# Performance work log

Measured on AMD Instinct MI355X. Metric: run time of the kernel, lower is better.

## Reference

```python
import jax, jax.numpy as jnp
import numpy as np

H = 128          # hidden / embed dim
NH = 4           # attention heads
HD = H // NH     # head dim = 32
MFD = 4          # missile feat dim
FOD = 15         # full obs dim
NEG_SLOPE = 0.01 # LeakyReLU default


def _gru(x_seq, h0, wih, whh, bih, bhh):
    # x_seq: [B,S,H], h0: [B,H]; torch GRU gate math
    def step(h, x):
        gi = x @ wih.T + bih            # [B,3H]
        gh = h @ whh.T + bhh
        i_r, i_z, i_n = jnp.split(gi, 3, axis=-1)
        h_r, h_z, h_n = jnp.split(gh, 3, axis=-1)
        r = jax.nn.sigmoid(i_r + h_r)
        z = jax.nn.sigmoid(i_z + h_z)
        n = jnp.tanh(i_n + r * h_n)
        h_new = (1.0 - z) * n + z * h
        return h_new, h_new
    h_last, outs = jax.lax.scan(step, h0, jnp.swapaxes(x_seq, 0, 1))
    return jnp.swapaxes(outs, 0, 1), h_last  # [B,S,H], [B,H]


def _ln(x, w, b, eps=1e-5):
    mu = jnp.mean(x, axis=-1, keepdims=True)
    var = jnp.var(x, axis=-1, keepdims=True)
    return (x - mu) * jax.lax.rsqrt(var + eps) * w + b


def setup_inputs() -> dict:
    key = jax.random.key(0)
    ks = jax.random.split(key, 24)
    B, S = 4096, 64
    s = 0.02
    p = {
        "obs": jax.random.normal(ks[0], (B, S, FOD), jnp.float32),
        "h0": jnp.zeros((1, B, H), jnp.float32),
        "enc_air_w": jax.random.normal(ks[1], (H, FOD)) * s,
        "enc_air_b": jnp.zeros((H,)),
        "enc_m_w": jax.random.normal(ks[2], (H, MFD)) * s,
        "enc_m_b": jnp.zeros((H,)),
        "gru_wih": jax.random.normal(ks[3], (3 * H, H)) * s,
        "gru_whh": jax.random.normal(ks[4], (3 * H, H)) * s,
        "gru_bih": jnp.zeros((3 * H,)),
        "gru_bhh": jnp.zeros((3 * H,)),
        "qln_w": jnp.ones((H,)), "qln_b": jnp.zeros((H,)),
        "kln_w": jnp.ones((H,)), "kln_b": jnp.zeros((H,)),
        "attn_in_w": jax.random.normal(ks[5], (3 * H, H)) * s,
        "attn_in_b": jnp.zeros((3 * H,)),
        "attn_out_w": jax.random.normal(ks[6], (H, H)) * s,
        "attn_out_b": jnp.zeros((H,)),
        "mlp0_w": jax.random.normal(ks[7], (H, H)) * s,
        "mlp0_b": jnp.zeros((H,)),
        "mlp1_w": jax.random.normal(ks[8], (H, H)) * s,
        "mlp1_b": jnp.zeros((H,)),
        "fco_w": jax.random.normal(ks[9], (1, H)) * s,
        "fco_b": jnp.zeros((1,)),
    }
    return {k: v.astype(jnp.float32) for k, v in p.items()}


def reference(obs, h0, enc_air_w, enc_air_b, enc_m_w, enc_m_b,
              gru_wih, gru_whh, gru_bih, gru_bhh,
              qln_w, qln_b, kln_w, kln_b,
              attn_in_w, attn_in_b, attn_out_w, attn_out_b,
              mlp0_w, mlp0_b, mlp1_w, mlp1_b, fco_w, fco_b):
    B, S, _ = obs.shape
    N = B * S
    # aircraft encoder + GRU with residual
    air_embed = obs @ enc_air_w.T + enc_air_b                      # [B,S,H]
    gru_out, h_last = _gru(air_embed, h0[0], gru_wih, gru_whh, gru_bih, gru_bhh)
    air_feat = (gru_out + air_embed).reshape(N, H)                 # [N,H]
    # missile encoders (shared weights, two missiles)
    m_raw = obs[..., :2 * MFD].reshape(N, 2, MFD)                  # [N,2,4]
    keys_raw = m_raw @ enc_m_w.T + enc_m_b                         # [N,2,H]
    # inactive-missile mask
    inactive = jnp.array([1.0, 0.0, 1.0, 0.0], obs.dtype)
    mask = jnp.all(jnp.isclose(m_raw, inactive, rtol=1e-5, atol=1e-8), axis=-1)  # [N,2]
    # layer norms
    q_n = _ln(air_feat[:, None, :], qln_w, qln_b)                  # [N,1,H]
    k_n = _ln(keys_raw, kln_w, kln_b)                              # [N,2,H]
    # multihead attention (1 query, 2 keys), values are raw keys
    wq, wk, wv = jnp.split(attn_in_w, 3, axis=0)
    bq, bk, bv = jnp.split(attn_in_b, 3, axis=0)
    q = (q_n @ wq.T + bq).reshape(N, 1, NH, HD)
    k = (k_n @ wk.T + bk).reshape(N, 2, NH, HD)
    v = (keys_raw @ wv.T + bv).reshape(N, 2, NH, HD)
    scores = jnp.einsum('nqhd,nkhd->nhqk', q, k) / jnp.sqrt(jnp.float32(HD))
    scores = scores + jnp.where(mask, -jnp.inf, 0.0)[:, None, None, :]
    attn = jax.nn.softmax(scores, axis=-1)                         # [N,NH,1,2]
    ctx = jnp.einsum('nhqk,nkhd->nqhd', attn, v).reshape(N, H)
    attn_out = ctx @ attn_out_w.T + attn_out_b                     # [N,H]
    attn_out = jnp.where(jnp.isnan(attn_out), 0.0, attn_out)       # nan_to_num guard
    combined = air_feat + attn_out
    # MLP head
    h1 = jax.nn.leaky_relu(combined @ mlp0_w.T + mlp0_b, NEG_SLOPE)
    h2 = jax.nn.leaky_relu(h1 @ mlp1_w.T + mlp1_b, NEG_SLOPE)
    val = h2 @ fco_w.T + fco_b                                     # [N,1]
    return val, h_last[None]
```

## Files before the change

kernel.cpp:

```cpp
#include <hip/hip_runtime.h>
#include <math.h>

#define B_   4096
#define S_   64
#define H_   128
#define N_   (B_*S_)

#define WS_WC    0
#define WS_BC    6144
#define WS_WAP   6528
#define WS_WQP   8576
#define WS_SQ    24960
#define WS_EQ    25088
#define WS_KC    25216
#define WS_EK1   25728
#define WS_SK    25856
#define WS_EK2   25984
#define WS_VC    26112
#define WS_VB    26624
#define WS_MV    26752
#define WS_QQ    26756
#define WS_QLIN  26772
#define WS_MBC   26776
#define WS_C0    26777
#define WS_PB    27392
#define WS_WO2T  (WS_PB + 4096)
#define WS_SROW  (WS_PB + 6784)
#define WS_EROW  (WS_PB + 6812)
#define WS_GB    60160
#define WS_AIR   92928

typedef __attribute__((ext_vector_type(8))) short bf16x8;
typedef __attribute__((ext_vector_type(4))) float f32x4;

__device__ __forceinline__ float dot4(float4 a, float4 b){
    return fmaf(a.x,b.x, fmaf(a.y,b.y, fmaf(a.z,b.z, a.w*b.w)));
}
__device__ __forceinline__ unsigned short f2bf(float f){
    union { float f; unsigned u; } v; v.f = f;
    unsigned r = v.u + 0x7FFF + ((v.u >> 16) & 1);
    return (unsigned short)(r >> 16);
}
__device__ __forceinline__ float bf2f(unsigned short u){
    union { unsigned u; float f; } v; v.u = ((unsigned)u) << 16;
    return v.f;
}

__global__ void precompute_kernel(
    const float* __restrict__ enc_air_w, const float* __restrict__ enc_air_b,
    const float* __restrict__ enc_m_w,  const float* __restrict__ enc_m_b,
    const float* __restrict__ gru_wih,  const float* __restrict__ gru_bih,
    const float* __restrict__ qln_w, const float* __restrict__ qln_b,
    const float* __restrict__ kln_w, const float* __restrict__ kln_b,
    const float* __restrict__ attn_in_w, const float* __restrict__ attn_in_b,
    const float* __restrict__ attn_out_w,
    const float* __restrict__ mlp0_w, const float* __restrict__ mlp1_w,
    float* __restrict__ ws)
{
    int i = blockIdx.x*blockDim.x + threadIdx.x;
    if (i < 6144) {
        int o = i>>4, f = i&15; float a = 0.f;
        if (f < 15) for (int k=0;k<128;k++) a = fmaf(gru_wih[o*128+k], enc_air_w[k*15+f], a);
        ws[WS_WC+i] = a;
    } else if (i < 6528) {
        int o = i-6144; float a = gru_bih[o];
        for (int k=0;k<128;k++) a = fmaf(gru_wih[o*128+k], enc_air_b[k], a);
        ws[WS_BC+o] = a;
    } else if (i < 8576) {
        int idx = i-6528; int j = idx>>4, f = idx&15;
        ws[WS_WAP+idx] = (f<15) ? enc_air_w[j*15+f] : 0.f;
    } else if (i < 24960) {
        int idx = i-8576; int o = idx>>7, j = idx&127;
        ws[WS_WQP+idx] = attn_in_w[o*128+j]*qln_w[j];
    } else if (i < 25088) {
        int o = i-24960; float a=0.f;
        for (int j=0;j<128;j++) a = fmaf(attn_in_w[o*128+j], qln_w[j], a);
        ws[WS_SQ+o]=a;
    } else if (i < 25216) {
        int o = i-25088; float a = attn_in_b[o];
        for (int j=0;j<128;j++) a = fmaf(attn_in_w[o*128+j], qln_b[j], a);
        ws[WS_EQ+o]=a;
    } else if (i < 25728) {
        int idx = i-25216; int o = idx>>2, f = idx&3; float a=0.f;
        for (int j=0;j<128;j++) a = fmaf(attn_in_w[(128+o)*128+j]*kln_w[j], enc_m_w[j*4+f], a);
        ws[WS_KC+idx]=a;
    } else if (i < 25856) {
        int o = i-25728; float a=0.f;
        for (int j=0;j<128;j++) a = fmaf(attn_in_w[(128+o)*128+j]*kln_w[j], enc_m_b[j], a);
        ws[WS_EK1+o]=a;
    } else if (i < 25984) {
        int o = i-25856; float a=0.f;
        for (int j=0;j<128;j++) a = fmaf(attn_in_w[(128+o)*128+j], kln_w[j], a);
        ws[WS_SK+o]=a;
    } else if (i < 26112) {
        int o = i-25984; float a = attn_in_b[128+o];
        for (int j=0;j<128;j++) a = fmaf(attn_in_w[(128+o)*128+j], kln_b[j], a);
        ws[WS_EK2+o]=a;
    } else if (i < 26624) {
        int idx = i-26112; int o = idx>>2, f = idx&3; float a=0.f;
        for (int j=0;j<128;j++) a = fmaf(attn_in_w[(256+o)*128+j], enc_m_w[j*4+f], a);
        ws[WS_VC+idx]=a;
    } else if (i < 26752) {
        int o = i-26624; float a = attn_in_b[256+o];
        for (int j=0;j<128;j++) a = fmaf(attn_in_w[(256+o)*128+j], enc_m_b[j], a);
        ws[WS_VB+o]=a;
    } else if (i < 26756) {
        int f = i-26752; float a=0.f;
        for (int j=0;j<128;j++) a += enc_m_w[j*4+f];
        ws[WS_MV+f]=a*(1.f/128.f);
    } else if (i < 26772) {
        int idx = i-26756; int a4 = idx>>2, b4 = idx&3; float a=0.f;
        for (int j=0;j<128;j++) a = fmaf(enc_m_w[j*4+a4], enc_m_w[j*4+b4], a);
        ws[WS_QQ+idx]=a*(1.f/128.f);
    } else if (i < 26776) {
        int f = i-26772; float a=0.f;
        for (int j=0;j<128;j++) a = fmaf(enc_m_b[j], enc_m_w[j*4+f], a);
        ws[WS_QLIN+f]=a*(2.f/128.f);
    } else if (i == 26776) {
        float a=0.f; for (int j=0;j<128;j++) a += enc_m_b[j];
        ws[WS_MBC]=a*(1.f/128.f);
    } else if (i == 26777) {
        float a=0.f; for (int j=0;j<128;j++) a = fmaf(enc_m_b[j], enc_m_b[j], a);
        ws[WS_C0]=a*(1.f/128.f);
    } else if (i >= 32768 && i < 98304) {
        int idx = i - 32768;
        int mm = idx>>14;
        if (mm >= 2) {
            int i8 = idx & 7, l = (idx>>3)&63, p = (idx>>9)&3, wv = (idx>>11)&7;
            int n = 16*wv + (l&15);
            int k = 32*p + ((l>>4)<<3) + i8;
            float v = (mm==2) ? mlp0_w[n*128+k] : mlp1_w[n*128+k];
            ((unsigned short*)(ws+WS_PB))[idx] = f2bf(v);
        }
    }
}

__global__ void pack_gru_kernel(const float* __restrict__ whh, float* __restrict__ ws)
{
    int idx = blockIdx.x*blockDim.x + threadIdx.x;
    int i8 = idx&7, l=(idx>>3)&63, w=(idx>>9)&7, f=idx>>12;
    int n = 16*w + (l&15);
    int k = ((l>>4)<<3) + i8;
    float v = 0.f;
    if (f < 5) {
        int kk = f*32 + k;
        if (kk < 128) v = whh[n*128 + kk];
        else { int kl = kk-128; if (kl<16) v = ws[WS_WC + n*16 + kl]; }
    } else if (f < 10) {
        int kk = (f-5)*32 + k;
        if (kk < 128) v = whh[(128+n)*128 + kk];
        else { int kl = kk-128; if (kl<16) v = ws[WS_WC + (128+n)*16 + kl]; }
    } else if (f < 14) {
        int kk = (f-10)*32 + k;
        v = whh[(256+n)*128 + kk];
    } else if (f == 14) {
        if (k < 16) v = ws[WS_WC + (256+n)*16 + k];
    } else {
        if (k < 16) v = ws[WS_WAP + n*16 + k];
    }
    ((unsigned short*)(ws+WS_GB))[idx] = f2bf(v);
}

__global__ void pack2_kernel(const float* __restrict__ wo, const float* __restrict__ bo,
                             float* __restrict__ ws)
{
    int i = blockIdx.x*blockDim.x + threadIdx.x;
    if (i < 4096) {
        int i8=i&7, l=(i>>3)&63, p=(i>>9)&3, ct=(i>>11)&1;
        int r = 16*ct + (l&15);
        int k = 32*p + ((l>>4)<<3) + i8;
        float v = 0.f;
        if (r < 28){
            int h = r/7, u = r - h*7;
            float a = 0.f;
            for (int d5=0; d5<32; d5++){
                int d = h*32 + d5;
                float c = (u<4) ? ws[WS_KC + d*4 + u]
                        : (u==4) ? ws[WS_EK1 + d]
                        : (u==5) ? ws[WS_SK + d]
                        :          ws[WS_EK2 + d];
                a = fmaf(c, ws[WS_WQP + d*128 + k], a);
            }
            v = a;
        }
        ((unsigned short*)(ws+WS_PB))[i] = f2bf(v);
    } else if (i < 4152) {
        int j = i - 4096; int r = j % 28; int era = j / 28;
        int h = r/7, u = r - h*7;
        float a = 0.f;
        for (int d5=0; d5<32; d5++){
            int d = h*32 + d5;
            float c = (u<4) ? ws[WS_KC + d*4 + u]
                    : (u==4) ? ws[WS_EK1 + d]
                    : (u==5) ? ws[WS_SK + d]
                    :          ws[WS_EK2 + d];
            a = fmaf(c, ws[(era ? WS_EQ : WS_SQ) + d], a);
        }
        ws[(era ? WS_EROW : WS_SROW) + r] = a;
    } else if (i >= 4224 && i < 6912) {
        int j = i - 4224; int c = j>>7, o = j&127;
        float a;
        if (c == 20) a = bo[o];
        else {
            int h = c/5, u = c - h*5;
            a = 0.f;
            for (int d5=0; d5<32; d5++){
                int d = h*32 + d5;
                float cv = (u<4) ? ws[WS_VC + d*4 + u] : ws[WS_VB + d];
                a = fmaf(wo[o*128 + d], cv, a);
            }
        }
        ws[WS_WO2T + c*128 + o] = a;
    }
}

__global__ void pack3_kernel(const float* __restrict__ mlp0_w, float* __restrict__ ws)
{
    int i = blockIdx.x*blockDim.x + threadIdx.x;
    int i8=i&7, l=(i>>3)&63, w=(i>>9)&7;
    int n = 16*w + (l&15);
    int c = ((l>>4)<<3) + i8;
    float v = 0.f;
    if (c < 21){
        float a = 0.f;
        const float* wo2 = ws + WS_WO2T + c*128;
        for (int o=0;o<128;o++) a = fmaf(mlp0_w[n*128+o], wo2[o], a);
        v = a;
    }
    ((unsigned short*)(ws+WS_PB))[4096 + i] = f2bf(v);
}

__global__ __launch_bounds__(512) void gru_kernel(
    const float* __restrict__ obs, const float* __restrict__ h0,
    const float* __restrict__ bhh, const float* __restrict__ ba,
    const float* __restrict__ ws,
    float* __restrict__ air, float* __restrict__ out)
{
    __shared__ __align__(16) unsigned short Abf[2][16*136];
    __shared__ __align__(16) unsigned short obs_lds[64*16*24];
    __shared__ __align__(16) unsigned short zero16[8];

    const int t = threadIdx.x;
    const int w = t>>6;
    const int l = t&63;
    const int quad = l>>4;
    const int col  = l&15;
    const int jj   = 16*w + col;
    const int row0 = blockIdx.x*16;

    const unsigned short* gb = (const unsigned short*)(ws + WS_GB);
    bf16x8 bf[16];
    #pragma unroll
    for (int f=0; f<16; f++) bf[f] = *(const bf16x8*)&gb[(f*8 + w)*512 + l*8];

    const float bcrt = ws[WS_BC+jj]     + bhh[jj];
    const float bczt = ws[WS_BC+128+jj] + bhh[128+jj];
    const float bcn  = ws[WS_BC+256+jj];
    const float bhn  = bhh[256+jj];
    const float baj  = ba[jj];

    float hreg[4];
    #pragma unroll
    for (int reg=0; reg<4; reg++)
        hreg[reg] = h0[(size_t)(row0+quad*4+reg)*128 + jj];

    if (t < 8) zero16[t] = 0;

    {
        int rr = t>>5, c0 = (t&31)*4;
        float4 hv = *(const float4*)&h0[(size_t)(row0+rr)*128 + c0];
        unsigned long long pk = (unsigned long long)f2bf(hv.x)
              | ((unsigned long long)f2bf(hv.y)<<16)
              | ((unsigned long long)f2bf(hv.z)<<32)
              | ((unsigned long long)f2bf(hv.w)<<48);
        *(unsigned long long*)&Abf[0][rr*136 + c0] = pk;
    }

    #pragma unroll
    for (int it=0; it<8; it++){
        int pair = it*128 + (t>>2);
        int sub  = t&3;
        int tok = pair>>6, s = pair&63;
        const float* op = &obs[((size_t)(row0+tok)*64 + s)*15 + sub*4];
        unsigned long long pk = 0;
        #pragma unroll
        for (int k=0;k<4;k++){
            int c = sub*4+k;
            float ov = (c<15) ? op[k] : 0.f;
            pk |= ((unsigned long long)f2bf(ov)) << (16*k);
        }
        *(unsigned long long*)&obs_lds[(s*16+tok)*24 + sub*4] = pk;
    }
    __syncthreads();

    for (int s=0; s<64; s++){
        const unsigned short* Ac = Abf[s&1];
        unsigned short*       An = Abf[(s+1)&1];

        bf16x8 a0 = *(const bf16x8*)&Ac[col*136 +  0 + quad*8];
        bf16x8 a1 = *(const bf16x8*)&Ac[col*136 + 32 + quad*8];
        bf16x8 a2 = *(const bf16x8*)&Ac[col*136 + 64 + quad*8];
        bf16x8 a3 = *(const bf16x8*)&Ac[col*136 + 96 + quad*8];
        const unsigned short* osrc = (quad<2)
            ? &obs_lds[(s*16+col)*24 + quad*8] : &zero16[0];
        bf16x8 a4 = *(const bf16x8*)osrc;

        f32x4 aR = {0.f,0.f,0.f,0.f};
        f32x4 aZ = {0.f,0.f,0.f,0.f};
        f32x4 aN = {0.f,0.f,0.f,0.f};
        f32x4 aG = {0.f,0.f,0.f,0.f};
        f32x4 aE = {0.f,0.f,0.f,0.f};
        aR = __builtin_amdgcn_mfma_f32_16x16x32_bf16(a0, bf[0],  aR, 0,0,0);
        aR = __builtin_amdgcn_mfma_f32_16x16x32_bf16(a1, bf[1],  aR, 0,0,0);
        aR = __builtin_amdgcn_mfma_f32_16x16x32_bf16(a2, bf[2],  aR, 0,0,0);
        aR = __builtin_amdgcn_mfma_f32_16x16x32_bf16(a3, bf[3],  aR, 0,0,0);
        aR = __builtin_amdgcn_mfma_f32_16x16x32_bf16(a4, bf[4],  aR, 0,0,0);
        aZ = __builtin_amdgcn_mfma_f32_16x16x32_bf16(a0, bf[5],  aZ, 0,0,0);
        aZ = __builtin_amdgcn_mfma_f32_16x16x32_bf16(a1, bf[6],  aZ, 0,0,0);
        aZ = __builtin_amdgcn_mfma_f32_16x16x32_bf16(a2, bf[7],  aZ, 0,0,0);
        aZ = __builtin_amdgcn_mfma_f32_16x16x32_bf16(a3, bf[8],  aZ, 0,0,0);
        aZ = __builtin_amdgcn_mfma_f32_16x16x32_bf16(a4, bf[9],  aZ, 0,0,0);
        aN = __builtin_amdgcn_mfma_f32_16x16x32_bf16(a0, bf[10], aN, 0,0,0);
        aN = __builtin_amdgcn_mfma_f32_16x16x32_bf16(a1, bf[11], aN, 0,0,0);
        aN = __builtin_amdgcn_mfma_f32_16x16x32_bf16(a2, bf[12], aN, 0,0,0);
        aN = __builtin_amdgcn_mfma_f32_16x16x32_bf16(a3, bf[13], aN, 0,0,0);
        aG = __builtin_amdgcn_mfma_f32_16x16x32_bf16(a4, bf[14], aG, 0,0,0);
        aE = __builtin_amdgcn_mfma_f32_16x16x32_bf16(a4, bf[15], aE, 0,0,0);

        #pragma unroll
        for (int reg=0; reg<4; reg++){
            int tok = quad*4 + reg;
            float rg = __builtin_amdgcn_rcpf(1.f + __expf(-(aR[reg] + bcrt)));
            float zg = __builtin_amdgcn_rcpf(1.f + __expf(-(aZ[reg] + bczt)));
            float nx = fmaf(rg, aN[reg] + bhn, aG[reg] + bcn);
            float e2 = __expf(2.f*nx);
            float ng = 1.f - 2.f*__builtin_amdgcn_rcpf(e2 + 1.f);
            float hn = fmaf(zg, hreg[reg]-ng, ng);
            hreg[reg] = hn;
            An[tok*136 + jj] = f2bf(hn);
            air[((size_t)(row0+tok)*64 + s)*128 + jj] = hn + (aE[reg] + baj);
        }
        if (s==63){
            #pragma unroll
            for (int reg=0; reg<4; reg++)
                out[(size_t)N_ + (size_t)(row0+quad*4+reg)*128 + jj] = hreg[reg];
        }
        asm volatile("s_waitcnt lgkmcnt(0)" ::: "memory");
        __builtin_amdgcn_s_barrier();
        __builtin_amdgcn_sched_barrier(0);
    }
}

__global__ __launch_bounds__(512) void attnmlp_kernel(
    const float* __restrict__ obs,
    const float* __restrict__ ws,
    const float* __restrict__ b0, const float* __restrict__ b1,
    const float* __restrict__ fcw, const float* __restrict__ fcb,
    const float* __restrict__ air, float* __restrict__ out)
{
    __shared__ __align__(16) unsigned short U_bf[64*168];
    __shared__ __align__(16) unsigned short H1_bf[64*136];
    __shared__ float praw[64*28];
    __shared__ float obs_m[64][8];
    __shared__ float mu_s[64], rs_s[64];
    __shared__ float kmu_s[64][2], krs_s[64][2];
    __shared__ int   kmask_s[64][2];

    const int t = threadIdx.x;
    const int w = t>>6;
    const int l = t&63;
    const int quad = l>>4;
    const int col  = l&15;
    const int jj   = 16*w + col;
    const int n0 = blockIdx.x*64;

    const unsigned short* pb = (const unsigned short*)(ws + WS_PB);

    {
        const int tok0 = t>>3, sub = t&7;
        const float* ap = &air[(size_t)(n0+tok0)*128 + sub*16];
        float sm = 0.f, s2 = 0.f;
        #pragma unroll
        for (int q4=0;q4<4;q4++){
            float4 xv = *(const float4*)&ap[q4*4];
            unsigned long long pk = (unsigned long long)f2bf(xv.x)
                  | ((unsigned long long)f2bf(xv.y)<<16)
                  | ((unsigned long long)f2bf(xv.z)<<32)
                  | ((unsigned long long)f2bf(xv.w)<<48);
            *(unsigned long long*)&U_bf[tok0*168 + sub*16 + q4*4] = pk;
            sm += xv.x+xv.y+xv.z+xv.w;
            s2 += fmaf(xv.x,xv.x, fmaf(xv.y,xv.y, fmaf(xv.z,xv.z, xv.w*xv.w)));
        }
        #pragma unroll
        for (int m=1;m<8;m<<=1){ sm += __shfl_xor(sm,m); s2 += __shfl_xor(s2,m); }
        if (sub==0){
            float mu = sm*(1.f/128.f);
            float var = s2*(1.f/128.f) - mu*mu;
            mu_s[tok0]=mu; rs_s[tok0]=rsqrtf(var+1e-5f);
        }
        if (sub<5){
            #pragma unroll
            for (int c=0;c<4;c++) U_bf[tok0*168 + 148 + sub*4 + c] = 0;
        }
        obs_m[tok0][sub] = obs[(size_t)(n0+tok0)*15 + sub];
    }
    if (t < 128){
        int rr = t>>1, mi = t&1;
        const float* mp = &obs[(size_t)(n0+rr)*15 + mi*4];
        float m0=mp[0], m1=mp[1], m2=mp[2], m3=mp[3];
        const float tol1 = 1e-8f + 1e-5f, tol0 = 1e-8f;
        kmask_s[rr][mi] = (fabsf(m0-1.f)<=tol1)&&(fabsf(m1)<=tol0)&&
                          (fabsf(m2-1.f)<=tol1)&&(fabsf(m3)<=tol0);
        float mv[4]={m0,m1,m2,m3};
        float mu = ws[WS_MBC];
        #pragma unroll
        for (int f=0;f<4;f++) mu = fmaf(ws[WS_MV+f], mv[f], mu);
        float e2 = ws[WS_C0];
        #pragma unroll
        for (int a4=0;a4<4;a4++){
            e2 = fmaf(ws[WS_QLIN+a4], mv[a4], e2);
            #pragma unroll
            for (int b4=0;b4<4;b4++) e2 = fmaf(ws[WS_QQ+a4*4+b4]*mv[a4], mv[b4], e2);
        }
        float var = e2 - mu*mu;
        kmu_s[rr][mi]=mu; krs_s[rr][mi]=rsqrtf(var+1e-5f);
    }
    __syncthreads();

    {
        const int tt = w>>1, ct = w&1;
        const int jA = ct*16 + col;
        f32x4 acc = {0.f,0.f,0.f,0.f};
        #pragma unroll
        for (int p=0;p<4;p++){
            bf16x8 a = *(const bf16x8*)&U_bf[(tt*16+col)*168 + p*32 + quad*8];
            bf16x8 b = *(const bf16x8*)&pb[((ct*4+p)*64 + l)*8];
            acc = __builtin_amdgcn_mfma_f32_16x16x32_bf16(a, b, acc, 0,0,0);
        }
        if (jA < 28){
            const float Sr = ws[WS_SROW + jA], Er = ws[WS_EROW + jA];
            #pragma unroll
            for (int reg=0;reg<4;reg++){
                int tok = tt*16 + quad*4 + reg;
                praw[tok*28 + jA] = fmaf(rs_s[tok], acc[reg] - mu_s[tok]*Sr, Er);
            }
        }
    }
    __syncthreads();

    if (t < 256){
        const int tok = t>>2, h = t&3;
        const float* pr = &praw[tok*28 + h*7];
        const float T0=pr[0],T1=pr[1],T2=pr[2],T3=pr[3],Pa=pr[4],Pb=pr[5],Pc=pr[6];
        const float4 m0v = *(const float4*)&obs_m[tok][0];
        const float4 m1v = *(const float4*)&obs_m[tok][4];
        const float scale = 0.17677669529663687f;
        float d0 = fmaf(T0,m0v.x, fmaf(T1,m0v.y, fmaf(T2,m0v.z, fmaf(T3,m0v.w, Pa))));
        float d1 = fmaf(T0,m1v.x, fmaf(T1,m1v.y, fmaf(T2,m1v.z, fmaf(T3,m1v.w, Pa))));
        float s0 = fmaf(krs_s[tok][0], d0 - kmu_s[tok][0]*Pb, Pc) * scale;
        float s1 = fmaf(krs_s[tok][1], d1 - kmu_s[tok][1]*Pb, Pc) * scale;
        int msk0 = kmask_s[tok][0], msk1 = kmask_s[tok][1];
        float a0, a1;
        if (msk0 && msk1){
            a0=0.f; a1=0.f;
            if (h==0) U_bf[tok*168 + 148] = 0;
        } else {
            if (h==0) U_bf[tok*168 + 148] = 0x3F80;
            if (msk0)      { a0=0.f; a1=1.f; }
            else if (msk1) { a0=1.f; a1=0.f; }
            else {
                float mx = fmaxf(s0,s1);
                float e0 = __expf(s0-mx), e1 = __expf(s1-mx);
                float inv = 1.f/(e0+e1);
                a0 = e0*inv; a1 = e1*inv;
            }
        }
        int cb = tok*168 + 128 + h*5;
        U_bf[cb+0] = f2bf(fmaf(a0, m0v.x, a1*m1v.x));
        U_bf[cb+1] = f2bf(fmaf(a0, m0v.y, a1*m1v.y));
        U_bf[cb+2] = f2bf(fmaf(a0, m0v.z, a1*m1v.z));
        U_bf[cb+3] = f2bf(fmaf(a0, m0v.w, a1*m1v.w));
        U_bf[cb+4] = f2bf(a0 + a1);
    }
    __syncthreads();

    {
        bf16x8 bfr[5];
        #pragma unroll
        for (int p=0;p<4;p++) bfr[p] = *(const bf16x8*)&pb[((2*32 + w*4 + p)*64 + l)*8];
        bfr[4] = *(const bf16x8*)&pb[4096 + (w*64 + l)*8];
        f32x4 acc[4];
        #pragma unroll
        for (int tt=0;tt<4;tt++) acc[tt] = (f32x4){0.f,0.f,0.f,0.f};
        #pragma unroll
        for (int p=0;p<5;p++){
            const int ko = p*32 + quad*8;
            #pragma unroll
            for (int tt=0;tt<4;tt++){
                bf16x8 a = *(const bf16x8*)&U_bf[(tt*16+col)*168 + ko];
                acc[tt] = __builtin_amdgcn_mfma_f32_16x16x32_bf16(a, bfr[p], acc[tt], 0,0,0);
            }
        }
        const float b0j = b0[jj];
        #pragma unroll
        for (int tt=0;tt<4;tt++){
            #pragma unroll
            for (int reg=0;reg<4;reg++){
                int tok = tt*16 + quad*4 + reg;
                float v = acc[tt][reg] + b0j;
                v = (v > 0.f) ? v : 0.01f*v;
                H1_bf[tok*136 + jj] = f2bf(v);
            }
        }
    }
    __syncthreads();

    {
        bf16x8 bfr[4];
        #pragma unroll
        for (int p=0;p<4;p++) bfr[p] = *(const bf16x8*)&pb[((3*32 + w*4 + p)*64 + l)*8];
        f32x4 acc[4];
        #pragma unroll
        for (int tt=0;tt<4;tt++) acc[tt] = (f32x4){0.f,0.f,0.f,0.f};
        #pragma unroll
        for (int p=0;p<4;p++){
            const int ko = p*32 + quad*8;
            #pragma unroll
            for (int tt=0;tt<4;tt++){
                bf16x8 a = *(const bf16x8*)&H1_bf[(tt*16+col)*136 + ko];
                acc[tt] = __builtin_amdgcn_mfma_f32_16x16x32_bf16(a, bfr[p], acc[tt], 0,0,0);
            }
        }
        const float b1j = b1[jj], fcj = fcw[jj];
        float pv[16];
        #pragma unroll
        for (int tt=0;tt<4;tt++){
            #pragma unroll
            for (int reg=0;reg<4;reg++){
                float v = acc[tt][reg] + b1j;
                v = (v > 0.f) ? v : 0.01f*v;
                pv[tt*4+reg] = v * fcj;
            }
        }
        #pragma unroll
        for (int m=1;m<16;m<<=1){
            #pragma unroll
            for (int q2=0;q2<16;q2++) pv[q2] += __shfl_xor(pv[q2], m);
        }
        if (col==0){
            #pragma unroll
            for (int tt=0;tt<4;tt++){
                #pragma unroll
                for (int reg=0;reg<4;reg++)
                    praw[(tt*16 + quad*4 + reg)*8 + w] = pv[tt*4+reg];
            }
        }
    }
    __syncthreads();

    if (t < 64){
        float a = fcb[0];
        #pragma unroll
        for (int k=0;k<8;k++) a += praw[t*8 + k];
        out[n0 + t] = a;
    }
}

extern "C" void kernel_launch(void* const* d_in, const int* in_sizes, int n_in,
                              void* d_out, int out_size, void* d_ws, size_t ws_size,
                              hipStream_t stream) {
    const float* obs       = (const float*)d_in[0];
    const float* h0        = (const float*)d_in[1];
    const float* enc_air_w = (const float*)d_in[2];
    const float* enc_air_b = (const float*)d_in[3];
    const float* enc_m_w   = (const float*)d_in[4];
    const float* enc_m_b   = (const float*)d_in[5];
    const float* gru_wih   = (const float*)d_in[6];
    const float* gru_whh   = (const float*)d_in[7];
    const float* gru_bih   = (const float*)d_in[8];
    const float* gru_bhh   = (const float*)d_in[9];
    const float* qln_w     = (const float*)d_in[10];
    const float* qln_b     = (const float*)d_in[11];
    const float* kln_w     = (const float*)d_in[12];
    const float* kln_b     = (const float*)d_in[13];
    const float* attn_in_w = (const float*)d_in[14];
    const float* attn_in_b = (const float*)d_in[15];
    const float* attn_out_w= (const float*)d_in[16];
    const float* attn_out_b= (const float*)d_in[17];
    const float* mlp0_w    = (const float*)d_in[18];
    const float* mlp0_b    = (const float*)d_in[19];
    const float* mlp1_w    = (const float*)d_in[20];
    const float* mlp1_b    = (const float*)d_in[21];
    const float* fco_w     = (const float*)d_in[22];
    const float* fco_b     = (const float*)d_in[23];
    float* out = (float*)d_out;
    float* ws  = (float*)d_ws;
    float* air = ws + WS_AIR;

    precompute_kernel<<<dim3(384), dim3(256), 0, stream>>>(
        enc_air_w, enc_air_b, enc_m_w, enc_m_b, gru_wih, gru_bih,
        qln_w, qln_b, kln_w, kln_b, attn_in_w, attn_in_b,
        attn_out_w, mlp0_w, mlp1_w, ws);

    pack_gru_kernel<<<dim3(256), dim3(256), 0, stream>>>(gru_whh, ws);
    pack2_kernel<<<dim3(27), dim3(256), 0, stream>>>(attn_out_w, attn_out_b, ws);
    pack3_kernel<<<dim3(16), dim3(256), 0, stream>>>(mlp0_w, ws);

    gru_kernel<<<dim3(256), dim3(512), 0, stream>>>(
        obs, h0, gru_bhh, enc_air_b, ws, air, out);

    attnmlp_kernel<<<dim3(N_/64), dim3(512), 0, stream>>>(
        obs, ws, mlp0_b, mlp1_b, fco_w, fco_b, air, out);
}
```

Baseline: 254.6 us.

## Store GRU air features as bf16 and halve attn/MLP tokens per block

The GRU kernel now writes the intermediate air tensor (N x 128) as bf16 instead of fp32, which halves global write and read traffic between the GRU and attention/MLP kernels. The attention/MLP kernel loads the bf16 values straight into LDS without converting, and now handles 32 tokens per block instead of 64, giving twice as many blocks. LayerNorm statistics are now computed from rounded bf16 values, which slightly changes precision. With 32 tokens per block, half the waves sit idle in the first projection stage and each MFMA stage does less work per wave.

```diff
diff --git a/kernel.cpp b/kernel.cpp
--- a/kernel.cpp
+++ b/kernel.cpp
@@ -29,6 +29,7 @@
 #define WS_EROW  (WS_PB + 6812)
 #define WS_GB    60160
 #define WS_AIR   92928
+#define TOKS     32
 
 typedef __attribute__((ext_vector_type(8))) short bf16x8;
 typedef __attribute__((ext_vector_type(4))) float f32x4;
@@ -234,7 +235,7 @@
     const float* __restrict__ obs, const float* __restrict__ h0,
     const float* __restrict__ bhh, const float* __restrict__ ba,
     const float* __restrict__ ws,
-    float* __restrict__ air, float* __restrict__ out)
+    unsigned short* __restrict__ air, float* __restrict__ out)
 {
     __shared__ __align__(16) unsigned short Abf[2][16*136];
     __shared__ __align__(16) unsigned short obs_lds[64*16*24];
@@ -338,7 +339,7 @@
             float hn = fmaf(zg, hreg[reg]-ng, ng);
             hreg[reg] = hn;
             An[tok*136 + jj] = f2bf(hn);
-            air[((size_t)(row0+tok)*64 + s)*128 + jj] = hn + (aE[reg] + baj);
+            air[((size_t)(row0+tok)*64 + s)*128 + jj] = f2bf(hn + (aE[reg] + baj));
         }
         if (s==63){
             #pragma unroll
@@ -356,15 +357,15 @@
     const float* __restrict__ ws,
     const float* __restrict__ b0, const float* __restrict__ b1,
     const float* __restrict__ fcw, const float* __restrict__ fcb,
-    const float* __restrict__ air, float* __restrict__ out)
+    const unsigned short* __restrict__ air, float* __restrict__ out)
 {
-    __shared__ __align__(16) unsigned short U_bf[64*168];
-    __shared__ __align__(16) unsigned short H1_bf[64*136];
-    __shared__ float praw[64*28];
-    __shared__ float obs_m[64][8];
-    __shared__ float mu_s[64], rs_s[64];
-    __shared__ float kmu_s[64][2], krs_s[64][2];
-    __shared__ int   kmask_s[64][2];
+    __shared__ __align__(16) unsigned short U_bf[TOKS*168];
+    __shared__ __align__(16) unsigned short H1_bf[TOKS*136];
+    __shared__ float praw[TOKS*28];
+    __shared__ float obs_m[TOKS][8];
+    __shared__ float mu_s[TOKS], rs_s[TOKS];
+    __shared__ float kmu_s[TOKS][2], krs_s[TOKS][2];
+    __shared__ int   kmask_s[TOKS][2];
 
     const int t = threadIdx.x;
     const int w = t>>6;
@@ -372,27 +373,26 @@
     const int quad = l>>4;
     const int col  = l&15;
     const int jj   = 16*w + col;
-    const int n0 = blockIdx.x*64;
+    const int n0 = blockIdx.x*TOKS;
 
     const unsigned short* pb = (const unsigned short*)(ws + WS_PB);
 
     {
-        const int tok0 = t>>3, sub = t&7;
-        const float* ap = &air[(size_t)(n0+tok0)*128 + sub*16];
+        const int tok0 = t>>4, sub = t&15;
+        const unsigned short* ap = &air[(size_t)(n0+tok0)*128 + sub*8];
+        uint4 xv = *(const uint4*)ap;
+        *(uint4*)&U_bf[tok0*168 + sub*8] = xv;
         float sm = 0.f, s2 = 0.f;
         #pragma unroll
         for (int q4=0;q4<4;q4++){
-            float4 xv = *(const float4*)&ap[q4*4];
-            unsigned long long pk = (unsigned long long)f2bf(xv.x)
-                  | ((unsigned long long)f2bf(xv.y)<<16)
-                  | ((unsigned long long)f2bf(xv.z)<<32)
-                  | ((unsigned long long)f2bf(xv.w)<<48);
-            *(unsigned long long*)&U_bf[tok0*168 + sub*16 + q4*4] = pk;
-            sm += xv.x+xv.y+xv.z+xv.w;
-            s2 += fmaf(xv.x,xv.x, fmaf(xv.y,xv.y, fmaf(xv.z,xv.z, xv.w*xv.w)));
-        }
-        #pragma unroll
-        for (int m=1;m<8;m<<=1){ sm += __shfl_xor(sm,m); s2 += __shfl_xor(s2,m); }
+            unsigned qv = ((const unsigned*)&xv)[q4];
+            float a = bf2f((unsigned short)(qv & 0xFFFF));
+            float b = bf2f((unsigned short)(qv >> 16));
+            sm += a + b;
+            s2 = fmaf(a,a, fmaf(b,b, s2));
+        }
+        #pragma unroll
+        for (int m=1;m<16;m<<=1){ sm += __shfl_xor(sm,m); s2 += __shfl_xor(s2,m); }
         if (sub==0){
             float mu = sm*(1.f/128.f);
             float var = s2*(1.f/128.f) - mu*mu;
@@ -402,9 +402,9 @@
             #pragma unroll
             for (int c=0;c<4;c++) U_bf[tok0*168 + 148 + sub*4 + c] = 0;
         }
-        obs_m[tok0][sub] = obs[(size_t)(n0+tok0)*15 + sub];
-    }
-    if (t < 128){
+        if (sub<8) obs_m[tok0][sub] = obs[(size_t)(n0+tok0)*15 + sub];
+    }
+    if (t < 64){
         int rr = t>>1, mi = t&1;
         const float* mp = &obs[(size_t)(n0+rr)*15 + mi*4];
         float m0=mp[0], m1=mp[1], m2=mp[2], m3=mp[3];
@@ -427,7 +427,7 @@
     }
     __syncthreads();
 
-    {
+    if (w < 4){
         const int tt = w>>1, ct = w&1;
         const int jA = ct*16 + col;
         f32x4 acc = {0.f,0.f,0.f,0.f};
@@ -448,7 +448,7 @@
     }
     __syncthreads();
 
-    if (t < 256){
+    if (t < TOKS*4){
         const int tok = t>>2, h = t&3;
         const float* pr = &praw[tok*28 + h*7];
         const float T0=pr[0],T1=pr[1],T2=pr[2],T3=pr[3],Pa=pr[4],Pb=pr[5],Pc=pr[6];
@@ -489,21 +489,21 @@
         #pragma unroll
         for (int p=0;p<4;p++) bfr[p] = *(const bf16x8*)&pb[((2*32 + w*4 + p)*64 + l)*8];
         bfr[4] = *(const bf16x8*)&pb[4096 + (w*64 + l)*8];
-        f32x4 acc[4];
-        #pragma unroll
-        for (int tt=0;tt<4;tt++) acc[tt] = (f32x4){0.f,0.f,0.f,0.f};
+        f32x4 acc[2];
+        #pragma unroll
+        for (int tt=0;tt<2;tt++) acc[tt] = (f32x4){0.f,0.f,0.f,0.f};
         #pragma unroll
         for (int p=0;p<5;p++){
             const int ko = p*32 + quad*8;
             #pragma unroll
-            for (int tt=0;tt<4;tt++){
+            for (int tt=0;tt<2;tt++){
                 bf16x8 a = *(const bf16x8*)&U_bf[(tt*16+col)*168 + ko];
                 acc[tt] = __builtin_amdgcn_mfma_f32_16x16x32_bf16(a, bfr[p], acc[tt], 0,0,0);
             }
         }
         const float b0j = b0[jj];
         #pragma unroll
-        for (int tt=0;tt<4;tt++){
+        for (int tt=0;tt<2;tt++){
             #pragma unroll
             for (int reg=0;reg<4;reg++){
                 int tok = tt*16 + quad*4 + reg;
@@ -519,22 +519,22 @@
         bf16x8 bfr[4];
         #pragma unroll
         for (int p=0;p<4;p++) bfr[p] = *(const bf16x8*)&pb[((3*32 + w*4 + p)*64 + l)*8];
-        f32x4 acc[4];
-        #pragma unroll
-        for (int tt=0;tt<4;tt++) acc[tt] = (f32x4){0.f,0.f,0.f,0.f};
+        f32x4 acc[2];
+        #pragma unroll
+        for (int tt=0;tt<2;tt++) acc[tt] = (f32x4){0.f,0.f,0.f,0.f};
         #pragma unroll
         for (int p=0;p<4;p++){
             const int ko = p*32 + quad*8;
             #pragma unroll
-            for (int tt=0;tt<4;tt++){
+            for (int tt=0;tt<2;tt++){
                 bf16x8 a = *(const bf16x8*)&H1_bf[(tt*16+col)*136 + ko];
                 acc[tt] = __builtin_amdgcn_mfma_f32_16x16x32_bf16(a, bfr[p], acc[tt], 0,0,0);
             }
         }
         const float b1j = b1[jj], fcj = fcw[jj];
-        float pv[16];
-        #pragma unroll
-        for (int tt=0;tt<4;tt++){
+        float pv[8];
+        #pragma unroll
+        for (int tt=0;tt<2;tt++){
             #pragma unroll
             for (int reg=0;reg<4;reg++){
                 float v = acc[tt][reg] + b1j;
@@ -545,11 +545,11 @@
         #pragma unroll
         for (int m=1;m<16;m<<=1){
             #pragma unroll
-            for (int q2=0;q2<16;q2++) pv[q2] += __shfl_xor(pv[q2], m);
+            for (int q2=0;q2<8;q2++) pv[q2] += __shfl_xor(pv[q2], m);
         }
         if (col==0){
             #pragma unroll
-            for (int tt=0;tt<4;tt++){
+            for (int tt=0;tt<2;tt++){
                 #pragma unroll
                 for (int reg=0;reg<4;reg++)
                     praw[(tt*16 + quad*4 + reg)*8 + w] = pv[tt*4+reg];
@@ -558,7 +558,7 @@
     }
     __syncthreads();
 
-    if (t < 64){
+    if (t < TOKS){
         float a = fcb[0];
         #pragma unroll
         for (int k=0;k<8;k++) a += praw[t*8 + k];
@@ -595,7 +595,7 @@
     const float* fco_b     = (const float*)d_in[23];
     float* out = (float*)d_out;
     float* ws  = (float*)d_ws;
-    float* air = ws + WS_AIR;
+    unsigned short* air = (unsigned short*)(ws + WS_AIR);
 
     precompute_kernel<<<dim3(384), dim3(256), 0, stream>>>(
         enc_air_w, enc_air_b, enc_m_w, enc_m_b, gru_wih, gru_bih,
@@ -609,6 +609,6 @@
     gru_kernel<<<dim3(256), dim3(512), 0, stream>>>(
         obs, h0, gru_bhh, enc_air_b, ws, air, out);
 
-    attnmlp_kernel<<<dim3(N_/64), dim3(512), 0, stream>>>(
+    attnmlp_kernel<<<dim3(N_/TOKS), dim3(512), 0, stream>>>(
         obs, ws, mlp0_b, mlp1_b, fco_w, fco_b, air, out);
 }
```

After: 251.4 us. No clear change (-1.2%).
